# Optimization experiments

Measured on AMD Instinct MI355X. Metric: run time of the kernel, lower is better.

The kernel has to match this reference:

```python
import jax, jax.numpy as jnp
import numpy as np

NUM_LAYER = 5
EMB = 256
N = 100000
E = 300000
SELF_LOOP_BOND = 4
BN_EPS = 1e-5


def setup_inputs() -> dict:
    key = jax.random.key(0)
    ks = jax.random.split(key, 16)
    f = lambda k, shape: jax.random.normal(k, shape, jnp.float32) * 0.02
    return {
        "x_atom": jax.random.randint(ks[0], (N,), 0, 120),
        "x_chir": jax.random.randint(ks[1], (N,), 0, 3),
        "edge_index": jax.random.randint(ks[2], (2, E), 0, N),
        "edge_bond": jax.random.randint(ks[3], (E,), 0, 4),
        "edge_dir": jax.random.randint(ks[4], (E,), 0, 3),
        "atom_emb": f(ks[5], (120, EMB)),
        "chir_emb": f(ks[6], (3, EMB)),
        "bond_embs": f(ks[7], (NUM_LAYER, 6, EMB)),
        "dir_embs": f(ks[8], (NUM_LAYER, 3, EMB)),
        "W1s": f(ks[9], (NUM_LAYER, 2 * EMB, EMB)),
        "b1s": f(ks[10], (NUM_LAYER, 2 * EMB)),
        "W2s": f(ks[11], (NUM_LAYER, EMB, 2 * EMB)),
        "b2s": f(ks[12], (NUM_LAYER, EMB)),
        "bn_w": jnp.ones((NUM_LAYER, EMB), jnp.float32),
        "bn_b": jnp.zeros((NUM_LAYER, EMB), jnp.float32),
    }


def reference(x_atom, x_chir, edge_index, edge_bond, edge_dir,
              atom_emb, chir_emb, bond_embs, dir_embs,
              W1s, b1s, W2s, b2s, bn_w, bn_b):
    n = x_atom.shape[0]
    src, dst = edge_index[0], edge_index[1]
    # add self loops (edge_attr = [4, 0] for each node)
    loop = jnp.arange(n)
    src_full = jnp.concatenate([src, loop])          # [E+N]
    dst_full = jnp.concatenate([dst, loop])          # [E+N]
    bond_full = jnp.concatenate([edge_bond, jnp.full((n,), SELF_LOOP_BOND, edge_bond.dtype)])
    dir_full = jnp.concatenate([edge_dir, jnp.zeros((n,), edge_dir.dtype)])

    # initial node features: atom + chirality embeddings
    h = atom_emb[x_atom] + chir_emb[x_chir]          # [N, EMB]

    for l in range(NUM_LAYER):
        # per-layer edge embeddings (bond type + bond direction)
        e_emb = bond_embs[l][bond_full] + dir_embs[l][dir_full]   # [E+N, EMB]
        # message = x_j + edge_attr; aggregate = scatter-add to dst
        msg = h[src_full] + e_emb                                  # gather
        agg = jax.ops.segment_sum(msg, dst_full, num_segments=n)  # scatter-add
        # update MLP: Linear(EMB->2EMB) -> ReLU -> Linear(2EMB->EMB)
        hmid = jax.nn.relu(agg @ W1s[l].T + b1s[l])                # [N, 2EMB]
        h2 = hmid @ W2s[l].T + b2s[l]                              # [N, EMB]
        # batch norm (training mode: batch statistics, biased variance)
        mean = h2.mean(axis=0)
        var = h2.var(axis=0)
        h2 = (h2 - mean) * jax.lax.rsqrt(var + BN_EPS) * bn_w[l] + bn_b[l]
        # relu on all but last layer; dropout with p=0 is identity
        if l < NUM_LAYER - 1:
            h2 = jax.nn.relu(h2)
        h = h2
    # JK == 'last'
    return h
```

## Files before the change

### kernel.cpp

```cpp
#include <hip/hip_runtime.h>

#define EMB 256
#define NLAYER 5
#define CHUNK 1024
#define NSLOT 64

typedef unsigned int u32;
typedef unsigned short u16;

typedef __bf16 bf16x8 __attribute__((ext_vector_type(8)));
typedef float f32x4 __attribute__((ext_vector_type(4)));

__device__ __forceinline__ float bf2f(u16 u) {
    union { u32 i; float f; } x; x.i = ((u32)u) << 16; return x.f;
}
__device__ __forceinline__ u16 f2bf(float f) {
    union { float f; u32 i; } x; x.f = f;
    u32 r = x.i + 0x7FFFu + ((x.i >> 16) & 1u);
    return (u16)(r >> 16);
}
__device__ __forceinline__ void unpack4(uint2 p, float* o) {
    union { u32 i; float f; } a, b, c, d;
    a.i = p.x << 16; b.i = p.x & 0xFFFF0000u;
    c.i = p.y << 16; d.i = p.y & 0xFFFF0000u;
    o[0] = a.f; o[1] = b.f; o[2] = c.f; o[3] = d.f;
}

__global__ void k_detect(const u32* __restrict__ bnw_raw, int* __restrict__ flag) {
    if (threadIdx.x == 0 && blockIdx.x == 0)
        *flag = (bnw_raw[0] == 0x3F803F80u) ? 1 : 0;
}

struct Cvt { const void* s; u16* d; int n; };
struct CvtTab { Cvt t[10]; };

__global__ void k_convert(CvtTab tab, const int* __restrict__ flag, int maxn) {
    int f = *flag;
    int stride = gridDim.x * blockDim.x;
    for (int i = blockIdx.x * blockDim.x + threadIdx.x; i < maxn; i += stride) {
        for (int j = 0; j < 10; j++) {
            if (i < tab.t[j].n) {
                u16 v;
                if (f) v = ((const u16*)tab.t[j].s)[i];
                else   v = f2bf(((const float*)tab.t[j].s)[i]);
                tab.t[j].d[i] = v;
            }
        }
    }
}

__global__ void k_zero(u32* p, int n) {
    int i = blockIdx.x * blockDim.x + threadIdx.x;
    if (i < n) p[i] = 0u;
}

__global__ void k_hist(const int* __restrict__ eidx, const int* __restrict__ ebond,
                       const int* __restrict__ edir,
                       u32* __restrict__ cnt, u32* __restrict__ cntb, u32* __restrict__ cntd, int E) {
    int e = blockIdx.x * blockDim.x + threadIdx.x;
    if (e >= E) return;
    int dst = eidx[E + e];
    atomicAdd(&cnt[dst], 1u);
    atomicAdd(&cntb[dst * 4 + ebond[e]], 1u);
    atomicAdd(&cntd[dst * 3 + edir[e]], 1u);
}

__global__ void k_chunksum(const u32* __restrict__ cnt, u32* __restrict__ partial, int N) {
    int b = blockIdx.x, t = threadIdx.x;
    int base = b * CHUNK + t * 4;
    u32 s = 0;
    for (int i = 0; i < 4; i++) { int idx = base + i; if (idx < N) s += cnt[idx]; }
    __shared__ u32 red[256];
    red[t] = s; __syncthreads();
    for (int o = 128; o > 0; o >>= 1) { if (t < o) red[t] += red[t + o]; __syncthreads(); }
    if (t == 0) partial[b] = red[0];
}

__global__ void k_scanpartial(u32* partial, u32* indptr, int nch, int N) {
    if (threadIdx.x == 0 && blockIdx.x == 0) {
        u32 run = 0;
        for (int i = 0; i < nch; i++) { u32 x = partial[i]; partial[i] = run; run += x; }
        indptr[N] = run;
    }
}

__global__ void k_chunkscan(const u32* __restrict__ cnt, const u32* __restrict__ partial,
                            u32* __restrict__ indptr, u32* __restrict__ fillp, int N) {
    int b = blockIdx.x, t = threadIdx.x;
    int base = b * CHUNK + t * 4;
    u32 c[4]; u32 tsum = 0;
    for (int i = 0; i < 4; i++) { int idx = base + i; c[i] = (idx < N) ? cnt[idx] : 0u; tsum += c[i]; }
    __shared__ u32 sc[256];
    sc[t] = tsum; __syncthreads();
    for (int o = 1; o < 256; o <<= 1) {
        u32 x = (t >= o) ? sc[t - o] : 0u;
        __syncthreads();
        sc[t] += x;
        __syncthreads();
    }
    u32 run = partial[b] + sc[t] - tsum;
    for (int i = 0; i < 4; i++) {
        int idx = base + i;
        if (idx < N) { indptr[idx] = run; fillp[idx] = run; }
        run += c[i];
    }
}

__global__ void k_fill(const int* __restrict__ eidx, u32* __restrict__ fillp,
                       u32* __restrict__ srcs, int E) {
    int e = blockIdx.x * blockDim.x + threadIdx.x;
    if (e >= E) return;
    int dst = eidx[E + e];
    u32 pos = atomicAdd(&fillp[dst], 1u);
    srcs[pos] = (u32)eidx[e];
}

__global__ void k_h0(const int* __restrict__ xa, const int* __restrict__ xc,
                     const u16* __restrict__ aemb, const u16* __restrict__ cemb,
                     u16* __restrict__ H, int N) {
    int wave = threadIdx.x >> 6, lane = threadIdx.x & 63;
    int v = blockIdx.x * 4 + wave;
    if (v >= N) return;
    int a = xa[v], c = xc[v];
    int c4 = lane * 4;
    uint2 pa = *(const uint2*)(aemb + (size_t)a * EMB + c4);
    uint2 pc = *(const uint2*)(cemb + (size_t)c * EMB + c4);
    float fa[4], fc[4];
    unpack4(pa, fa); unpack4(pc, fc);
    ushort4 ov;
    ov.x = f2bf(fa[0] + fc[0]); ov.y = f2bf(fa[1] + fc[1]);
    ov.z = f2bf(fa[2] + fc[2]); ov.w = f2bf(fa[3] + fc[3]);
    *(ushort4*)(H + (size_t)v * EMB + c4) = ov;
}

__global__ void k_scatter(const u16* __restrict__ H, const u32* __restrict__ indptr,
                          const u32* __restrict__ srcs,
                          const u32* __restrict__ cntb, const u32* __restrict__ cntd,
                          const u16* __restrict__ bemb, const u16* __restrict__ demb,
                          const float* __restrict__ scsh, int relu,
                          u16* __restrict__ AGG, int N) {
    int wave = threadIdx.x >> 6, lane = threadIdx.x & 63;
    int v = blockIdx.x * 4 + wave;
    if (v >= N) return;
    int c4 = lane * 4;
    float sc[4] = {1.f, 1.f, 1.f, 1.f}, sh[4] = {0.f, 0.f, 0.f, 0.f};
    if (scsh) {
        float4 s0 = *(const float4*)(scsh + c4);
        float4 s1 = *(const float4*)(scsh + 256 + c4);
        sc[0] = s0.x; sc[1] = s0.y; sc[2] = s0.z; sc[3] = s0.w;
        sh[0] = s1.x; sh[1] = s1.y; sh[2] = s1.z; sh[3] = s1.w;
    }
    float acc[4] = {0.f, 0.f, 0.f, 0.f};
    u32 beg = indptr[v], end = indptr[v + 1];
    for (u32 e = beg; e < end; e++) {
        u32 s = srcs[e];
        uint2 p = *(const uint2*)(H + (size_t)s * EMB + c4);
        float f[4]; unpack4(p, f);
        for (int i = 0; i < 4; i++) {
            float y = f[i] * sc[i] + sh[i];
            if (relu) y = fmaxf(y, 0.f);
            acc[i] += y;
        }
    }
    {
        uint2 p = *(const uint2*)(H + (size_t)v * EMB + c4);
        float f[4]; unpack4(p, f);
        for (int i = 0; i < 4; i++) {
            float y = f[i] * sc[i] + sh[i];
            if (relu) y = fmaxf(y, 0.f);
            acc[i] += y;
        }
    }
    float cb[5];
    cb[0] = (float)cntb[v * 4 + 0]; cb[1] = (float)cntb[v * 4 + 1];
    cb[2] = (float)cntb[v * 4 + 2]; cb[3] = (float)cntb[v * 4 + 3]; cb[4] = 1.f;
    float cd[3];
    cd[0] = (float)cntd[v * 3 + 0] + 1.f; cd[1] = (float)cntd[v * 3 + 1]; cd[2] = (float)cntd[v * 3 + 2];
    for (int b = 0; b < 5; b++) {
        uint2 p = *(const uint2*)(bemb + b * EMB + c4);
        float f[4]; unpack4(p, f);
        for (int i = 0; i < 4; i++) acc[i] += cb[b] * f[i];
    }
    for (int d = 0; d < 3; d++) {
        uint2 p = *(const uint2*)(demb + d * EMB + c4);
        float f[4]; unpack4(p, f);
        for (int i = 0; i < 4; i++) acc[i] += cd[d] * f[i];
    }
    ushort4 ov;
    ov.x = f2bf(acc[0]); ov.y = f2bf(acc[1]); ov.z = f2bf(acc[2]); ov.w = f2bf(acc[3]);
    *(ushort4*)(AGG + (size_t)v * EMB + c4) = ov;
}

#define KP1 264

__global__ __launch_bounds__(256, 2) void k_gemm1(
    const u16* __restrict__ A, const u16* __restrict__ W1, const u16* __restrict__ bias,
    u16* __restrict__ HM, int M) {
    __shared__ __align__(16) u16 As[64 * KP1];
    int m0 = blockIdx.x * 64;
    int t = threadIdx.x;
    int wave = t >> 6, lane = t & 63;
    int lr = lane & 15, quad = lane >> 4;

    for (int it = 0; it < 8; it++) {
        int ci = t + it * 256;
        int r = ci >> 5, kc = (ci & 31) * 8;
        int gr = m0 + r; if (gr > M - 1) gr = M - 1;
        *(uint4*)(As + r * KP1 + kc) = *(const uint4*)(A + (size_t)gr * 256 + kc);
    }
    __syncthreads();

    int nbase = wave * 128;
    f32x4 acc[4][8];
    for (int i = 0; i < 4; i++)
        for (int j = 0; j < 8; j++)
            acc[i][j] = (f32x4){0.f, 0.f, 0.f, 0.f};

    for (int ks = 0; ks < 256; ks += 32) {
        bf16x8 af[4], bfr[8];
        for (int i = 0; i < 4; i++)
            af[i] = *(const bf16x8*)(As + (i * 16 + lr) * KP1 + ks + quad * 8);
        for (int j = 0; j < 8; j++)
            bfr[j] = *(const bf16x8*)(W1 + (size_t)(nbase + j * 16 + lr) * 256 + ks + quad * 8);
        for (int i = 0; i < 4; i++)
            for (int j = 0; j < 8; j++)
                acc[i][j] = __builtin_amdgcn_mfma_f32_16x16x32_bf16(af[i], bfr[j], acc[i][j], 0, 0, 0);
    }
    for (int j = 0; j < 8; j++) {
        int gn = nbase + j * 16 + lr;
        float bv = bf2f(bias[gn]);
        for (int i = 0; i < 4; i++) {
            int mbase = m0 + i * 16 + quad * 4;
            for (int r = 0; r < 4; r++) {
                int gm = mbase + r;
                if (gm < M)
                    HM[(size_t)gm * 512 + gn] = f2bf(fmaxf(acc[i][j][r] + bv, 0.f));
            }
        }
    }
}

#define KP2 520

__global__ __launch_bounds__(256, 2) void k_gemm2(
    const u16* __restrict__ A, const u16* __restrict__ W2, const u16* __restrict__ bias,
    u16* __restrict__ C, float* __restrict__ S, int M) {
    __shared__ __align__(16) u16 As[64 * KP2];
    int m0 = blockIdx.x * 64;
    int t = threadIdx.x;
    int wave = t >> 6, lane = t & 63;
    int lr = lane & 15, quad = lane >> 4;

    for (int it = 0; it < 16; it++) {
        int ci = t + it * 256;
        int r = ci >> 6, kc = (ci & 63) * 8;
        int gr = m0 + r; if (gr > M - 1) gr = M - 1;
        *(uint4*)(As + r * KP2 + kc) = *(const uint4*)(A + (size_t)gr * 512 + kc);
    }
    __syncthreads();

    int nbase = wave * 64;
    f32x4 acc[4][4];
    for (int i = 0; i < 4; i++)
        for (int j = 0; j < 4; j++)
            acc[i][j] = (f32x4){0.f, 0.f, 0.f, 0.f};

    for (int ks = 0; ks < 512; ks += 32) {
        bf16x8 af[4], bfr[4];
        for (int i = 0; i < 4; i++)
            af[i] = *(const bf16x8*)(As + (i * 16 + lr) * KP2 + ks + quad * 8);
        for (int j = 0; j < 4; j++)
            bfr[j] = *(const bf16x8*)(W2 + (size_t)(nbase + j * 16 + lr) * 512 + ks + quad * 8);
        for (int i = 0; i < 4; i++)
            for (int j = 0; j < 4; j++)
                acc[i][j] = __builtin_amdgcn_mfma_f32_16x16x32_bf16(af[i], bfr[j], acc[i][j], 0, 0, 0);
    }
    float* Sslot = S + (size_t)(blockIdx.x & (NSLOT - 1)) * 512;
    for (int j = 0; j < 4; j++) {
        int gn = nbase + j * 16 + lr;
        float bv = bf2f(bias[gn]);
        float s = 0.f, q = 0.f;
        for (int i = 0; i < 4; i++) {
            int mbase = m0 + i * 16 + quad * 4;
            for (int r = 0; r < 4; r++) {
                int gm = mbase + r;
                if (gm < M) {
                    float v = acc[i][j][r] + bv;
                    C[(size_t)gm * 256 + gn] = f2bf(v);
                    s += v; q += v * v;
                }
            }
        }
        s += __shfl_xor(s, 16, 64); s += __shfl_xor(s, 32, 64);
        q += __shfl_xor(q, 16, 64); q += __shfl_xor(q, 32, 64);
        if (quad == 0) {
            atomicAdd(&Sslot[gn], s);
            atomicAdd(&Sslot[256 + gn], q);
        }
    }
}

__global__ void k_finalize(const float* __restrict__ S, const u16* __restrict__ bnw,
                           const u16* __restrict__ bnb, float* __restrict__ scsh, float invN) {
    int c = threadIdx.x;
    float sum = 0.f, sq = 0.f;
    for (int i = 0; i < NSLOT; i++) {
        sum += S[(size_t)i * 512 + c];
        sq  += S[(size_t)i * 512 + 256 + c];
    }
    float mean = sum * invN;
    float var = sq * invN - mean * mean;
    var = fmaxf(var, 0.f);
    float inv = rsqrtf(var + 1e-5f);
    float sc = bf2f(bnw[c]) * inv;
    scsh[c] = sc;
    scsh[256 + c] = bf2f(bnb[c]) - mean * sc;
}

__global__ void k_out(const u16* __restrict__ H2, const float* __restrict__ scsh,
                      void* __restrict__ out, const int* __restrict__ flag, int N) {
    int wave = threadIdx.x >> 6, lane = threadIdx.x & 63;
    int v = blockIdx.x * 4 + wave;
    if (v >= N) return;
    int c4 = lane * 4;
    float4 s0 = *(const float4*)(scsh + c4);
    float4 s1 = *(const float4*)(scsh + 256 + c4);
    uint2 p = *(const uint2*)(H2 + (size_t)v * EMB + c4);
    float f[4]; unpack4(p, f);
    float o0 = f[0] * s0.x + s1.x;
    float o1 = f[1] * s0.y + s1.y;
    float o2 = f[2] * s0.z + s1.z;
    float o3 = f[3] * s0.w + s1.w;
    if (*flag) {
        ushort4 ov;
        ov.x = f2bf(o0); ov.y = f2bf(o1); ov.z = f2bf(o2); ov.w = f2bf(o3);
        *(ushort4*)((u16*)out + (size_t)v * EMB + c4) = ov;
    } else {
        float4 ov = make_float4(o0, o1, o2, o3);
        *(float4*)((float*)out + (size_t)v * EMB + c4) = ov;
    }
}

extern "C" void kernel_launch(void* const* d_in, const int* in_sizes, int n_in,
                              void* d_out, int out_size, void* d_ws, size_t ws_size,
                              hipStream_t stream) {
    const int* x_atom = (const int*)d_in[0];
    const int* x_chir = (const int*)d_in[1];
    const int* eidx   = (const int*)d_in[2];
    const int* ebond  = (const int*)d_in[3];
    const int* edir   = (const int*)d_in[4];

    const int N = in_sizes[0];
    const int E = in_sizes[3];

    char* p = (char*)d_ws;
    size_t off = 0;
    auto alloc = [&](size_t bytes) -> void* {
        void* r = p + off;
        off += bytes;
        off = (off + 255) & ~(size_t)255;
        return r;
    };
    u16* X   = (u16*)alloc((size_t)N * EMB * 2);
    u16* Y   = (u16*)alloc((size_t)N * EMB * 2);
    u16* HM  = (u16*)alloc((size_t)N * 512 * 2);
    const size_t statsWords = (size_t)NLAYER * NSLOT * 512;
    u32* cz  = (u32*)alloc(((size_t)8 * N + statsWords) * 4);
    u32* cnt  = cz;
    u32* cntb = cz + N;
    u32* cntd = cz + 5 * (size_t)N;
    float* stats5 = (float*)(cz + 8 * (size_t)N);
    u32* indptr = (u32*)alloc((size_t)(N + 1) * 4);
    u32* fillp  = (u32*)alloc((size_t)N * 4);
    u32* srcs   = (u32*)alloc((size_t)E * 4);
    u32* partial = (u32*)alloc(256 * 4);
    float* scsh  = (float*)alloc(512 * 4);
    int* flag    = (int*)alloc(256);

    int csz[10] = {120 * EMB, 3 * EMB, NLAYER * 6 * EMB, NLAYER * 3 * EMB,
                   NLAYER * 512 * EMB, NLAYER * 512, NLAYER * EMB * 512, NLAYER * EMB,
                   NLAYER * EMB, NLAYER * EMB};
    u16* cbuf[10];
    for (int j = 0; j < 10; j++) cbuf[j] = (u16*)alloc((size_t)csz[j] * 2);
    u16* atom_emb  = cbuf[0];
    u16* chir_emb  = cbuf[1];
    u16* bond_embs = cbuf[2];
    u16* dir_embs  = cbuf[3];
    u16* W1s = cbuf[4];
    u16* b1s = cbuf[5];
    u16* W2s = cbuf[6];
    u16* b2s = cbuf[7];
    u16* bnw = cbuf[8];
    u16* bnb = cbuf[9];

    const int nodeBlocks = (N + 3) / 4;
    const int nch = (N + CHUNK - 1) / CHUNK;

    k_detect<<<1, 64, 0, stream>>>((const u32*)d_in[13], flag);
    {
        CvtTab tab;
        int maxn = 0;
        for (int j = 0; j < 10; j++) {
            tab.t[j].s = d_in[5 + j];
            tab.t[j].d = cbuf[j];
            tab.t[j].n = csz[j];
            if (csz[j] > maxn) maxn = csz[j];
        }
        k_convert<<<(maxn + 255) / 256, 256, 0, stream>>>(tab, flag, maxn);
    }

    {
        size_t z = 8 * (size_t)N + statsWords;
        k_zero<<<(int)((z + 255) / 256), 256, 0, stream>>>(cz, (int)z);
    }
    k_hist<<<(E + 255) / 256, 256, 0, stream>>>(eidx, ebond, edir, cnt, cntb, cntd, E);
    k_chunksum<<<nch, 256, 0, stream>>>(cnt, partial, N);
    k_scanpartial<<<1, 64, 0, stream>>>(partial, indptr, nch, N);
    k_chunkscan<<<nch, 256, 0, stream>>>(cnt, partial, indptr, fillp, N);
    k_fill<<<(E + 255) / 256, 256, 0, stream>>>(eidx, fillp, srcs, E);

    k_h0<<<nodeBlocks, 256, 0, stream>>>(x_atom, x_chir, atom_emb, chir_emb, X, N);

    u16* H = X;
    u16* A = Y;
    const int mTiles64 = (N + 63) / 64;
    for (int l = 0; l < NLAYER; l++) {
        const u16* bemb = bond_embs + (size_t)l * 6 * EMB;
        const u16* demb = dir_embs + (size_t)l * 3 * EMB;
        const u16* W1 = W1s + (size_t)l * 512 * EMB;
        const u16* B1 = b1s + (size_t)l * 512;
        const u16* W2 = W2s + (size_t)l * EMB * 512;
        const u16* B2 = b2s + (size_t)l * EMB;
        float* stats = stats5 + (size_t)l * NSLOT * 512;

        k_scatter<<<nodeBlocks, 256, 0, stream>>>(H, indptr, srcs, cntb, cntd, bemb, demb,
                                                  (l == 0) ? nullptr : scsh, (l == 0) ? 0 : 1,
                                                  A, N);
        k_gemm1<<<mTiles64, 256, 0, stream>>>(A, W1, B1, HM, N);
        k_gemm2<<<mTiles64, 256, 0, stream>>>(HM, W2, B2, A, stats, N);
        k_finalize<<<1, 256, 0, stream>>>(stats, bnw + (size_t)l * EMB, bnb + (size_t)l * EMB,
                                          scsh, 1.0f / (float)N);
        u16* tmp = H; H = A; A = tmp;
    }

    k_out<<<nodeBlocks, 256, 0, stream>>>(H, scsh, d_out, flag, N);
}
```

Before: 1.473 ms.

## Fuse both MLP GEMMs into one kernel keeping hidden activations in LDS

```diff
diff --git a/kernel.cpp b/kernel.cpp
--- a/kernel.cpp
+++ b/kernel.cpp
@@ -191,12 +191,16 @@
     *(ushort4*)(AGG + (size_t)v * EMB + c4) = ov;
 }
 
-#define KP1 264
-
-__global__ __launch_bounds__(256, 2) void k_gemm1(
-    const u16* __restrict__ A, const u16* __restrict__ W1, const u16* __restrict__ bias,
-    u16* __restrict__ HM, int M) {
-    __shared__ __align__(16) u16 As[64 * KP1];
+#define KAS 272
+#define KHM 144
+#define KEP 264
+
+__global__ __launch_bounds__(256) void k_mlp(
+    const u16* __restrict__ A, const u16* __restrict__ W1, const u16* __restrict__ B1,
+    const u16* __restrict__ W2, const u16* __restrict__ B2,
+    u16* __restrict__ C, float* __restrict__ S, int M) {
+    __shared__ __align__(16) u16 As[64 * KAS];
+    __shared__ __align__(16) u16 HMb[64 * KHM];
     int m0 = blockIdx.x * 64;
     int t = threadIdx.x;
     int wave = t >> 6, lane = t & 63;
@@ -206,88 +210,70 @@
         int ci = t + it * 256;
         int r = ci >> 5, kc = (ci & 31) * 8;
         int gr = m0 + r; if (gr > M - 1) gr = M - 1;
-        *(uint4*)(As + r * KP1 + kc) = *(const uint4*)(A + (size_t)gr * 256 + kc);
+        *(uint4*)(As + r * KAS + kc) = *(const uint4*)(A + (size_t)gr * 256 + kc);
     }
     __syncthreads();
 
-    int nbase = wave * 128;
-    f32x4 acc[4][8];
-    for (int i = 0; i < 4; i++)
-        for (int j = 0; j < 8; j++)
-            acc[i][j] = (f32x4){0.f, 0.f, 0.f, 0.f};
-
-    for (int ks = 0; ks < 256; ks += 32) {
-        bf16x8 af[4], bfr[8];
-        for (int i = 0; i < 4; i++)
-            af[i] = *(const bf16x8*)(As + (i * 16 + lr) * KP1 + ks + quad * 8);
-        for (int j = 0; j < 8; j++)
-            bfr[j] = *(const bf16x8*)(W1 + (size_t)(nbase + j * 16 + lr) * 256 + ks + quad * 8);
-        for (int i = 0; i < 4; i++)
-            for (int j = 0; j < 8; j++)
-                acc[i][j] = __builtin_amdgcn_mfma_f32_16x16x32_bf16(af[i], bfr[j], acc[i][j], 0, 0, 0);
-    }
-    for (int j = 0; j < 8; j++) {
-        int gn = nbase + j * 16 + lr;
-        float bv = bf2f(bias[gn]);
-        for (int i = 0; i < 4; i++) {
-            int mbase = m0 + i * 16 + quad * 4;
-            for (int r = 0; r < 4; r++) {
-                int gm = mbase + r;
-                if (gm < M)
-                    HM[(size_t)gm * 512 + gn] = f2bf(fmaxf(acc[i][j][r] + bv, 0.f));
-            }
-        }
-    }
-}
-
-#define KP2 520
-
-__global__ __launch_bounds__(256, 2) void k_gemm2(
-    const u16* __restrict__ A, const u16* __restrict__ W2, const u16* __restrict__ bias,
-    u16* __restrict__ C, float* __restrict__ S, int M) {
-    __shared__ __align__(16) u16 As[64 * KP2];
-    int m0 = blockIdx.x * 64;
-    int t = threadIdx.x;
-    int wave = t >> 6, lane = t & 63;
-    int lr = lane & 15, quad = lane >> 4;
-
-    for (int it = 0; it < 16; it++) {
-        int ci = t + it * 256;
-        int r = ci >> 6, kc = (ci & 63) * 8;
-        int gr = m0 + r; if (gr > M - 1) gr = M - 1;
-        *(uint4*)(As + r * KP2 + kc) = *(const uint4*)(A + (size_t)gr * 512 + kc);
-    }
-    __syncthreads();
-
-    int nbase = wave * 64;
-    f32x4 acc[4][4];
+    f32x4 acc2[4][4];
     for (int i = 0; i < 4; i++)
         for (int j = 0; j < 4; j++)
-            acc[i][j] = (f32x4){0.f, 0.f, 0.f, 0.f};
-
-    for (int ks = 0; ks < 512; ks += 32) {
-        bf16x8 af[4], bfr[4];
+            acc2[i][j] = (f32x4){0.f, 0.f, 0.f, 0.f};
+    int n0 = wave * 64;
+
+    for (int wc = 0; wc < 4; wc++) {
+        int nb1 = wc * 128 + wave * 32;
+        f32x4 acc1[4][2];
         for (int i = 0; i < 4; i++)
-            af[i] = *(const bf16x8*)(As + (i * 16 + lr) * KP2 + ks + quad * 8);
-        for (int j = 0; j < 4; j++)
-            bfr[j] = *(const bf16x8*)(W2 + (size_t)(nbase + j * 16 + lr) * 512 + ks + quad * 8);
-        for (int i = 0; i < 4; i++)
+            for (int jj = 0; jj < 2; jj++)
+                acc1[i][jj] = (f32x4){0.f, 0.f, 0.f, 0.f};
+        for (int ks = 0; ks < 256; ks += 32) {
+            bf16x8 af[4], bfr[2];
+            for (int i = 0; i < 4; i++)
+                af[i] = *(const bf16x8*)(As + (i * 16 + lr) * KAS + ks + quad * 8);
+            for (int jj = 0; jj < 2; jj++)
+                bfr[jj] = *(const bf16x8*)(W1 + (size_t)(nb1 + jj * 16 + lr) * 256 + ks + quad * 8);
+            for (int i = 0; i < 4; i++)
+                for (int jj = 0; jj < 2; jj++)
+                    acc1[i][jj] = __builtin_amdgcn_mfma_f32_16x16x32_bf16(af[i], bfr[jj], acc1[i][jj], 0, 0, 0);
+        }
+        if (wc) __syncthreads();
+        for (int jj = 0; jj < 2; jj++) {
+            int lc = wave * 32 + jj * 16 + lr;
+            float bv = bf2f(B1[wc * 128 + lc]);
+            for (int i = 0; i < 4; i++) {
+                int row = i * 16 + quad * 4;
+                for (int r = 0; r < 4; r++)
+                    HMb[(row + r) * KHM + lc] = f2bf(fmaxf(acc1[i][jj][r] + bv, 0.f));
+            }
+        }
+        __syncthreads();
+        for (int ks = 0; ks < 128; ks += 32) {
+            bf16x8 af[4], bfr[4];
+            for (int i = 0; i < 4; i++)
+                af[i] = *(const bf16x8*)(HMb + (i * 16 + lr) * KHM + ks + quad * 8);
             for (int j = 0; j < 4; j++)
-                acc[i][j] = __builtin_amdgcn_mfma_f32_16x16x32_bf16(af[i], bfr[j], acc[i][j], 0, 0, 0);
-    }
+                bfr[j] = *(const bf16x8*)(W2 + (size_t)(n0 + j * 16 + lr) * 512 + wc * 128 + ks + quad * 8);
+            for (int i = 0; i < 4; i++)
+                for (int j = 0; j < 4; j++)
+                    acc2[i][j] = __builtin_amdgcn_mfma_f32_16x16x32_bf16(af[i], bfr[j], acc2[i][j], 0, 0, 0);
+        }
+    }
+
+    __syncthreads();
     float* Sslot = S + (size_t)(blockIdx.x & (NSLOT - 1)) * 512;
     for (int j = 0; j < 4; j++) {
-        int gn = nbase + j * 16 + lr;
-        float bv = bf2f(bias[gn]);
+        int gn = n0 + j * 16 + lr;
+        float bv = bf2f(B2[gn]);
         float s = 0.f, q = 0.f;
         for (int i = 0; i < 4; i++) {
-            int mbase = m0 + i * 16 + quad * 4;
+            int rbase = i * 16 + quad * 4;
             for (int r = 0; r < 4; r++) {
-                int gm = mbase + r;
-                if (gm < M) {
-                    float v = acc[i][j][r] + bv;
-                    C[(size_t)gm * 256 + gn] = f2bf(v);
+                if (m0 + rbase + r < M) {
+                    float v = acc2[i][j][r] + bv;
+                    As[(rbase + r) * KEP + gn] = f2bf(v);
                     s += v; q += v * v;
+                } else {
+                    As[(rbase + r) * KEP + gn] = 0;
                 }
             }
         }
@@ -297,6 +283,13 @@
             atomicAdd(&Sslot[gn], s);
             atomicAdd(&Sslot[256 + gn], q);
         }
+    }
+    __syncthreads();
+    for (int it = 0; it < 8; it++) {
+        int ci = t + it * 256;
+        int r = ci >> 5, c8 = (ci & 31) * 8;
+        if (m0 + r < M)
+            *(uint4*)(C + (size_t)(m0 + r) * 256 + c8) = *(const uint4*)(As + r * KEP + c8);
     }
 }
 
@@ -363,7 +356,6 @@
     };
     u16* X   = (u16*)alloc((size_t)N * EMB * 2);
     u16* Y   = (u16*)alloc((size_t)N * EMB * 2);
-    u16* HM  = (u16*)alloc((size_t)N * 512 * 2);
     const size_t statsWords = (size_t)NLAYER * NSLOT * 512;
     u32* cz  = (u32*)alloc(((size_t)8 * N + statsWords) * 4);
     u32* cnt  = cz;
@@ -436,11 +428,12 @@
         k_scatter<<<nodeBlocks, 256, 0, stream>>>(H, indptr, srcs, cntb, cntd, bemb, demb,
                                                   (l == 0) ? nullptr : scsh, (l == 0) ? 0 : 1,
                                                   A, N);
-        k_gemm1<<<mTiles64, 256, 0, stream>>>(A, W1, B1, HM, N);
-        k_gemm2<<<mTiles64, 256, 0, stream>>>(HM, W2, B2, A, stats, N);
+        u16* Cdst = (A == X) ? Y : X;
+        k_mlp<<<mTiles64, 256, 0, stream>>>(A, W1, B1, W2, B2, Cdst, stats, N);
         k_finalize<<<1, 256, 0, stream>>>(stats, bnw + (size_t)l * EMB, bnb + (size_t)l * EMB,
                                           scsh, 1.0f / (float)N);
-        u16* tmp = H; H = A; A = tmp;
+        H = Cdst;
+        A = (Cdst == X) ? Y : X;
     }
 
     k_out<<<nodeBlocks, 256, 0, stream>>>(H, scsh, d_out, flag, N);
```

New measurement: 1.326 ms. 10.0% less time.
